# Performance work log

Measured on AMD Instinct MI355X. Metric: run time of the kernel, lower is better.

The kernel has to match this reference:

```python
import jax, jax.numpy as jnp
import numpy as np

B, L, C, H, HH, NL, O = 4096, 512, 8, 64, 128, 3, 1  # batch, time length, input/hidden/hidden_hidden chans, layers, out


def _lin(k, i, o):
    s = 1.0 / np.sqrt(i)
    return jax.random.uniform(k, (i, o), jnp.float32, -s, s)


def setup_inputs():
    key = jax.random.key(0)
    ks = jax.random.split(key, 8)
    return {
        "coeffs": jax.random.normal(ks[0], (B, L - 1, 4 * C), jnp.float32) * 0.1,
        "W_init": _lin(ks[1], C, H), "b_init": jnp.zeros((H,), jnp.float32),
        "W_in": _lin(ks[2], H, HH), "b_in": jnp.zeros((HH,), jnp.float32),
        "W_h": jnp.stack([_lin(ks[3 + i], HH, HH) for i in range(NL - 1)]),
        "b_h": jnp.zeros((NL - 1, HH), jnp.float32),
        "W_out": _lin(ks[5], HH, C * H), "b_out": jnp.zeros((C * H,), jnp.float32),
        "W_read": _lin(ks[6], H, O), "b_read": jnp.zeros((O,), jnp.float32),
    }


def _cde_func(z, W_in, b_in, W_h, b_h, W_out, b_out):
    # CDEFunc MLP: (B,H) -> (B,H,C)
    h = jax.nn.relu(z @ W_in + b_in)
    for i in range(W_h.shape[0]):
        h = jax.nn.relu(h @ W_h[i] + b_h[i])
    f = jnp.tanh(h @ W_out + b_out)
    return f.reshape(z.shape[0], H, C)


def reference(coeffs, W_init, b_init, W_in, b_in, W_h, b_h, W_out, b_out, W_read, b_read):
    # torchcde.CubicSpline coeffs layout: cat([a, b, two_c, three_d], dim=-1)
    a, bb, two_c, three_d = jnp.split(coeffs, 4, axis=-1)  # each (B, L-1, C)
    # X(interval[0]) = a of the first segment (fractional part 0)
    z = a[:, 0, :] @ W_init + b_init  # (B, H)
    # grid_points = arange(L); step size h = 1 between consecutive grid points
    bs = jnp.moveaxis(bb, 1, 0)       # (L-1, B, C)
    cs = jnp.moveaxis(two_c, 1, 0)
    ds = jnp.moveaxis(three_d, 1, 0)

    def step(z, seg):
        bn, cn, dn = seg
        deriv = lambda frac: bn + (cn + dn * frac) * frac  # dX/dt within segment
        g = lambda zz, dX: jnp.einsum(
            'bhc,bc->bh', _cde_func(zz, W_in, b_in, W_h, b_h, W_out, b_out), dX)
        third = jnp.float32(1.0 / 3.0)
        # torchdiffeq 'rk4' fixed-grid solver = Kutta's 3/8 rule (rk4_alt_step_func), h=1
        k1 = g(z, deriv(0.0))
        k2 = g(z + k1 * third, deriv(third))
        k3 = g(z + (k2 - k1 * third), deriv(2.0 * third))
        k4 = g(z + (k1 - k2 + k3), deriv(1.0))
        z = z + (k1 + 3.0 * (k2 + k3) + k4) * jnp.float32(0.125)
        return z, None

    zT, _ = jax.lax.scan(step, z, (bs, cs, ds))  # final hidden state z(T)
    return zT @ W_read + b_read  # (B, O)
```

## Files before the change

### kernel.cpp

```cpp
#include <hip/hip_runtime.h>
#include <stdint.h>

typedef short s16x8 __attribute__((ext_vector_type(8)));
typedef float f32x4 __attribute__((ext_vector_type(4)));

#define LSEG 511

static __device__ __forceinline__ uint32_t cvt_pk_bf16(float lo, float hi) {
  uint32_t r;
  asm("v_cvt_pk_bf16_f32 %0, %1, %2" : "=v"(r) : "v"(lo), "v"(hi));
  return r;
}
static __device__ __forceinline__ unsigned short f2bf(float f) {
  union { float f; uint32_t u; } v; v.f = f;
  uint32_t r = (v.u + 0x7FFFu + ((v.u >> 16) & 1u)) >> 16;
  return (unsigned short)r;
}
static __device__ __forceinline__ float dpp_xor8(float x) {
  return __int_as_float(__builtin_amdgcn_update_dpp(
      0, __float_as_int(x), 0x128, 0xF, 0xF, false));
}

__global__ __attribute__((amdgpu_flat_work_group_size(512, 512),
                          amdgpu_waves_per_eu(2, 2)))
void cde_kernel(
    const float* __restrict__ coeffs,
    const float* __restrict__ W_init, const float* __restrict__ b_init,
    const float* __restrict__ W_in,  const float* __restrict__ b_in,
    const float* __restrict__ W_h,   const float* __restrict__ b_h,
    const float* __restrict__ W_out, const float* __restrict__ b_out,
    const float* __restrict__ W_read,const float* __restrict__ b_read,
    float* __restrict__ out)
{
  __shared__ __align__(16) char H1mem[16 * 256];
  __shared__ __align__(16) char H2mem[16 * 256];
  __shared__ __align__(16) char Xmem[16 * 128];
  __shared__ float dx2[4][2][16][4];

  const int tid  = threadIdx.x;
  const int w    = tid >> 6;
  const int lane = tid & 63;
  const int lr   = lane & 15;
  const int lk   = lane >> 4;
  const int lc   = lr & 7;
  const int hp   = lr >> 3;
  const int b0   = blockIdx.x * 16;
  const int h_own = 8*w + lc;

  const float TS = 2.8853900817779268f;

  s16x8 Win_f[2], Wh0_f[4], Wh1_f[4], Wout_f[4][4];
  const int wc = 16*w + lr;
  #pragma unroll
  for (int kq = 0; kq < 2; ++kq)
    #pragma unroll
    for (int e = 0; e < 8; ++e)
      Win_f[kq][e] = (short)f2bf(W_in[(32*kq + 8*lk + e)*128 + wc]);
  #pragma unroll
  for (int kq = 0; kq < 4; ++kq)
    #pragma unroll
    for (int e = 0; e < 8; ++e) {
      Wh0_f[kq][e] = (short)f2bf(W_h[(32*kq + 8*lk + e)*128 + wc]);
      Wh1_f[kq][e] = (short)f2bf(W_h[16384 + (32*kq + 8*lk + e)*128 + wc]);
    }
  #pragma unroll
  for (int kq = 0; kq < 4; ++kq)
    #pragma unroll
    for (int nt = 0; nt < 4; ++nt) {
      const int ch = 64*w + 8*lc + 2*nt + hp;
      #pragma unroll
      for (int e = 0; e < 8; ++e)
        Wout_f[kq][nt][e] = (short)f2bf(W_out[(32*kq + 8*lk + e)*512 + ch] * TS);
    }
  const float binv = b_in[wc];
  const float bh0v = b_h[wc];
  const float bh1v = b_h[128 + wc];
  const f32x4 bin4 = {binv, binv, binv, binv};
  const f32x4 bh04 = {bh0v, bh0v, bh0v, bh0v};
  const f32x4 bh14 = {bh1v, bh1v, bh1v, bh1v};
  f32x4 bout4[4];
  #pragma unroll
  for (int nt = 0; nt < 4; ++nt) {
    const float b = b_out[64*w + 8*lc + 2*nt + hp] * TS;
    bout4[nt] = (f32x4){b, b, b, b};
  }

  const int r2  = (lr >> 2) & 1;
  const int vbHe = lr*256 + (((lk ^ lr) & 3) << 4) + (r2 << 6);
  const int vbHo = lr*256 + (((lk ^ lr) & 3) << 4) + ((1 ^ r2) << 6);
  const int vbX0 = lr*128 + ((lk ^ (lr & 7)) << 4);
  const int vbX1 = vbX0 ^ 64;
  int wbH[4];
  #pragma unroll
  for (int r = 0; r < 4; ++r) {
    const int row = 4*lk + r;
    wbH[r] = row*256 + ((((2*w + (lr >> 3)) ^ (row & 7)) << 4)) + ((lr & 7) << 1);
  }
  int wbX[2];
  #pragma unroll
  for (int j = 0; j < 2; ++j) {
    const int ro = 4*lk + 2*hp + j;
    wbX[j] = ro*128 + (((w ^ (ro & 7)) << 4)) + (lc << 1);
  }
  const int dbx = hp*256 + lk*64;

  float z0[2], zfin[2], k1r[2], k2r[2];
  {
    float Wi[8];
    #pragma unroll
    for (int c = 0; c < 8; ++c) Wi[c] = W_init[c*64 + h_own];
    const float bi = b_init[h_own];
    #pragma unroll
    for (int j = 0; j < 2; ++j) {
      const int ro = 4*lk + 2*hp + j;
      const float* a0r = &coeffs[(size_t)(b0 + ro) * (LSEG*32)];
      float s = bi;
      #pragma unroll
      for (int c = 0; c < 8; ++c) s = fmaf(a0r[c], Wi[c], s);
      z0[j] = s; zfin[j] = 0.f; k1r[j] = 0.f; k2r[j] = 0.f;
      *(unsigned short*)(Xmem + wbX[j]) = f2bf(s);
    }
  }

  float cf_b = 0.f, cf_c = 0.f, cf_d = 0.f;
  const int crow = 2*w + (lane >> 5);
  const int ccc  = (lane >> 2) & 7;
  const bool cact = (lane & 3) == 0;
  if (cact) {
    const float* cp = &coeffs[(size_t)(b0 + crow)*(LSEG*32)];
    cf_b = cp[8+ccc]; cf_c = cp[16+ccc]; cf_d = cp[24+ccc];
  }
  __syncthreads();

  #pragma unroll 1
  for (int t = 0; t < LSEG; ++t) {
    #pragma unroll
    for (int s = 0; s < 4; ++s) {
      if (s == 0 && cact) {
        const float third = 1.f/3.f, two3 = 2.f/3.f;
        const int dxo = (ccc & 1)*256 + crow*16 + (ccc >> 1)*4;
        *(float*)((char*)dx2 + dxo)        = cf_b;
        *(float*)((char*)dx2 + dxo + 512)  = fmaf(fmaf(cf_d, third, cf_c), third, cf_b);
        *(float*)((char*)dx2 + dxo + 1024) = fmaf(fmaf(cf_d, two3, cf_c), two3, cf_b);
        *(float*)((char*)dx2 + dxo + 1536) = cf_b + cf_c + cf_d;
        if (t + 1 < LSEG) {
          const float* cp = &coeffs[((size_t)(b0 + crow)*LSEG + (t+1))*32];
          cf_b = cp[8+ccc]; cf_c = cp[16+ccc]; cf_d = cp[24+ccc];
        }
      }
      {
        s16x8 a0 = *(const s16x8*)(Xmem + vbX0);
        s16x8 a1 = *(const s16x8*)(Xmem + vbX1);
        __builtin_amdgcn_s_setprio(1);
        f32x4 acc;
        acc = __builtin_amdgcn_mfma_f32_16x16x32_bf16(a0, Win_f[0], bin4, 0, 0, 0);
        acc = __builtin_amdgcn_mfma_f32_16x16x32_bf16(a1, Win_f[1], acc, 0, 0, 0);
        __builtin_amdgcn_s_setprio(0);
        #pragma unroll
        for (int r = 0; r < 4; ++r) {
          float v = fmaxf(acc[r], 0.f);
          *(unsigned short*)(H1mem + wbH[r]) = (unsigned short)cvt_pk_bf16(v, v);
        }
      }
      __syncthreads();

      {
        s16x8 a0 = *(const s16x8*)(H1mem + vbHe);
        s16x8 a1 = *(const s16x8*)(H1mem + vbHo);
        s16x8 a2 = *(const s16x8*)(H1mem + vbHe + 128);
        s16x8 a3 = *(const s16x8*)(H1mem + vbHo + 128);
        __builtin_amdgcn_s_setprio(1);
        f32x4 acc0, acc1 = {};
        acc0 = __builtin_amdgcn_mfma_f32_16x16x32_bf16(a0, Wh0_f[0], bh04, 0, 0, 0);
        acc1 = __builtin_amdgcn_mfma_f32_16x16x32_bf16(a1, Wh0_f[1], acc1, 0, 0, 0);
        acc0 = __builtin_amdgcn_mfma_f32_16x16x32_bf16(a2, Wh0_f[2], acc0, 0, 0, 0);
        acc1 = __builtin_amdgcn_mfma_f32_16x16x32_bf16(a3, Wh0_f[3], acc1, 0, 0, 0);
        __builtin_amdgcn_s_setprio(0);
        f32x4 acc = acc0 + acc1;
        #pragma unroll
        for (int r = 0; r < 4; ++r) {
          float v = fmaxf(acc[r], 0.f);
          *(unsigned short*)(H2mem + wbH[r]) = (unsigned short)cvt_pk_bf16(v, v);
        }
      }
      __syncthreads();

      {
        s16x8 a0 = *(const s16x8*)(H2mem + vbHe);
        s16x8 a1 = *(const s16x8*)(H2mem + vbHo);
        s16x8 a2 = *(const s16x8*)(H2mem + vbHe + 128);
        s16x8 a3 = *(const s16x8*)(H2mem + vbHo + 128);
        __builtin_amdgcn_s_setprio(1);
        f32x4 acc0, acc1 = {};
        acc0 = __builtin_amdgcn_mfma_f32_16x16x32_bf16(a0, Wh1_f[0], bh14, 0, 0, 0);
        acc1 = __builtin_amdgcn_mfma_f32_16x16x32_bf16(a1, Wh1_f[1], acc1, 0, 0, 0);
        acc0 = __builtin_amdgcn_mfma_f32_16x16x32_bf16(a2, Wh1_f[2], acc0, 0, 0, 0);
        acc1 = __builtin_amdgcn_mfma_f32_16x16x32_bf16(a3, Wh1_f[3], acc1, 0, 0, 0);
        __builtin_amdgcn_s_setprio(0);
        f32x4 acc = acc0 + acc1;
        #pragma unroll
        for (int r = 0; r < 4; ++r) {
          float v = fmaxf(acc[r], 0.f);
          *(unsigned short*)(H1mem + wbH[r]) = (unsigned short)cvt_pk_bf16(v, v);
        }
      }
      __syncthreads();

      {
        f32x4 dxv[4];
        #pragma unroll
        for (int r = 0; r < 4; ++r)
          dxv[r] = *(const f32x4*)((const char*)dx2 + dbx + s*512 + r*16);
        s16x8 a0 = *(const s16x8*)(H1mem + vbHe);
        s16x8 a1 = *(const s16x8*)(H1mem + vbHo);
        s16x8 a2 = *(const s16x8*)(H1mem + vbHe + 128);
        s16x8 a3 = *(const s16x8*)(H1mem + vbHo + 128);
        __builtin_amdgcn_s_setprio(1);
        f32x4 acc[4];
        #pragma unroll
        for (int nt = 0; nt < 4; ++nt)
          acc[nt] = __builtin_amdgcn_mfma_f32_16x16x32_bf16(a0, Wout_f[0][nt], bout4[nt], 0, 0, 0);
        #pragma unroll
        for (int nt = 0; nt < 4; ++nt)
          acc[nt] = __builtin_amdgcn_mfma_f32_16x16x32_bf16(a1, Wout_f[1][nt], acc[nt], 0, 0, 0);
        #pragma unroll
        for (int nt = 0; nt < 4; ++nt)
          acc[nt] = __builtin_amdgcn_mfma_f32_16x16x32_bf16(a2, Wout_f[2][nt], acc[nt], 0, 0, 0);
        #pragma unroll
        for (int nt = 0; nt < 4; ++nt)
          acc[nt] = __builtin_amdgcn_mfma_f32_16x16x32_bf16(a3, Wout_f[3][nt], acc[nt], 0, 0, 0);
        __builtin_amdgcn_s_setprio(0);
        float sums[4];
        #pragma unroll
        for (int r = 0; r < 4; ++r) {
          float sum = 0.f;
          #pragma unroll
          for (int nt = 0; nt < 4; ++nt) {
            float e2 = __builtin_amdgcn_exp2f(acc[nt][r]);
            float rr = __builtin_amdgcn_rcpf(e2 + 1.f);
            float tv = fmaf(-2.f, rr, 1.f);
            sum = fmaf(tv, dxv[r][nt], sum);
          }
          sums[r] = sum + dpp_xor8(sum);
        }
        #pragma unroll
        for (int j = 0; j < 2; ++j) {
          const float sum = sums[2*hp + j];
          float znext;
          if (s == 0) {
            k1r[j] = sum;
            zfin[j] = fmaf(0.125f, sum, z0[j]);
            znext   = fmaf(1.f/3.f, sum, z0[j]);
          } else if (s == 1) {
            k2r[j] = sum;
            zfin[j] = fmaf(0.375f, sum, zfin[j]);
            znext   = z0[j] + sum - (1.f/3.f)*k1r[j];
          } else if (s == 2) {
            zfin[j] = fmaf(0.375f, sum, zfin[j]);
            znext   = z0[j] + k1r[j] - k2r[j] + sum;
          } else {
            zfin[j] = fmaf(0.125f, sum, zfin[j]);
            znext   = zfin[j];
            z0[j]   = zfin[j];
          }
          *(unsigned short*)(Xmem + wbX[j]) = (unsigned short)cvt_pk_bf16(znext, znext);
        }
      }
      __syncthreads();
    }
  }

  float* ZF = (float*)H1mem;
  #pragma unroll
  for (int j = 0; j < 2; ++j)
    ZF[(4*lk + 2*hp + j)*64 + h_own] = z0[j];
  __syncthreads();
  if (tid < 16) {
    float acc = b_read[0];
    for (int h = 0; h < 64; ++h) acc = fmaf(ZF[tid*64 + h], W_read[h], acc);
    out[b0 + tid] = acc;
  }
}

extern "C" void kernel_launch(void* const* d_in, const int* in_sizes, int n_in,
                              void* d_out, int out_size, void* d_ws, size_t ws_size,
                              hipStream_t stream) {
  const float* coeffs = (const float*)d_in[0];
  const float* W_init = (const float*)d_in[1];
  const float* b_init = (const float*)d_in[2];
  const float* W_in   = (const float*)d_in[3];
  const float* b_in   = (const float*)d_in[4];
  const float* W_h    = (const float*)d_in[5];
  const float* b_h    = (const float*)d_in[6];
  const float* W_out  = (const float*)d_in[7];
  const float* b_out  = (const float*)d_in[8];
  const float* W_read = (const float*)d_in[9];
  const float* b_read = (const float*)d_in[10];
  float* out = (float*)d_out;

  cde_kernel<<<dim3(256), dim3(512), 0, stream>>>(
      coeffs, W_init, b_init, W_in, b_in, W_h, b_h, W_out, b_out,
      W_read, b_read, out);
}
```

Baseline: 2.828 ms.

## Swap MFMA operand order to produce transposed outputs with packed LDS stores

Swaps the A/B operands of every MFMA so weights become the row operand and activations the column operand, which transposes the output fragment layout. Each lane now holds four consecutive hidden channels of one batch row, so it writes one packed 8-byte LDS store instead of four scalar 2-byte stores, and the dX reads shrink to a single vector load. The Wout column mapping, bias vectors, swizzles and dX buffer layout are rearranged to match. The cross-lane reduction moves from a DPP xor-8 to a shuffle xor-32. RK4 state per lane grows from two to four values, with duplicated work in the upper lanes.

```diff
diff --git a/kernel.cpp b/kernel.cpp
--- a/kernel.cpp
+++ b/kernel.cpp
@@ -3,6 +3,7 @@
 
 typedef short s16x8 __attribute__((ext_vector_type(8)));
 typedef float f32x4 __attribute__((ext_vector_type(4)));
+typedef uint32_t u32x2 __attribute__((ext_vector_type(2)));
 
 #define LSEG 511
 
@@ -15,10 +16,6 @@
   union { float f; uint32_t u; } v; v.f = f;
   uint32_t r = (v.u + 0x7FFFu + ((v.u >> 16) & 1u)) >> 16;
   return (unsigned short)r;
-}
-static __device__ __forceinline__ float dpp_xor8(float x) {
-  return __int_as_float(__builtin_amdgcn_update_dpp(
-      0, __float_as_int(x), 0x128, 0xF, 0xF, false));
 }
 
 __global__ __attribute__((amdgpu_flat_work_group_size(512, 512),
@@ -35,17 +32,14 @@
   __shared__ __align__(16) char H1mem[16 * 256];
   __shared__ __align__(16) char H2mem[16 * 256];
   __shared__ __align__(16) char Xmem[16 * 128];
-  __shared__ float dx2[4][2][16][4];
+  __shared__ float dx2[4][16][8];
 
   const int tid  = threadIdx.x;
   const int w    = tid >> 6;
   const int lane = tid & 63;
   const int lr   = lane & 15;
   const int lk   = lane >> 4;
-  const int lc   = lr & 7;
-  const int hp   = lr >> 3;
   const int b0   = blockIdx.x * 16;
-  const int h_own = 8*w + lc;
 
   const float TS = 2.8853900817779268f;
 
@@ -67,58 +61,52 @@
   for (int kq = 0; kq < 4; ++kq)
     #pragma unroll
     for (int nt = 0; nt < 4; ++nt) {
-      const int ch = 64*w + 8*lc + 2*nt + hp;
+      const int ch = (8*w + 2*nt + ((lr >> 2) & 1))*8 + (lr & 3) + 4*((lr >> 3) & 1);
       #pragma unroll
       for (int e = 0; e < 8; ++e)
         Wout_f[kq][nt][e] = (short)f2bf(W_out[(32*kq + 8*lk + e)*512 + ch] * TS);
     }
-  const float binv = b_in[wc];
-  const float bh0v = b_h[wc];
-  const float bh1v = b_h[128 + wc];
-  const f32x4 bin4 = {binv, binv, binv, binv};
-  const f32x4 bh04 = {bh0v, bh0v, bh0v, bh0v};
-  const f32x4 bh14 = {bh1v, bh1v, bh1v, bh1v};
-  f32x4 bout4[4];
-  #pragma unroll
-  for (int nt = 0; nt < 4; ++nt) {
-    const float b = b_out[64*w + 8*lc + 2*nt + hp] * TS;
-    bout4[nt] = (f32x4){b, b, b, b};
-  }
-
-  const int r2  = (lr >> 2) & 1;
-  const int vbHe = lr*256 + (((lk ^ lr) & 3) << 4) + (r2 << 6);
-  const int vbHo = lr*256 + (((lk ^ lr) & 3) << 4) + ((1 ^ r2) << 6);
+  f32x4 bin4, bh04, bh14, bout4[4];
+  #pragma unroll
+  for (int r = 0; r < 4; ++r) {
+    bin4[r] = b_in[16*w + 4*lk + r];
+    bh04[r] = b_h[16*w + 4*lk + r];
+    bh14[r] = b_h[128 + 16*w + 4*lk + r];
+  }
+  #pragma unroll
+  for (int nt = 0; nt < 4; ++nt)
+    #pragma unroll
+    for (int r = 0; r < 4; ++r)
+      bout4[nt][r] = b_out[(8*w + 2*nt + (lk & 1))*8 + 4*(lk >> 1) + r] * TS;
+
+  int vb[4];
+  #pragma unroll
+  for (int kq = 0; kq < 4; ++kq)
+    vb[kq] = lr*256 + (((4*kq + lk) ^ (lr & 7)) << 4);
   const int vbX0 = lr*128 + ((lk ^ (lr & 7)) << 4);
   const int vbX1 = vbX0 ^ 64;
-  int wbH[4];
-  #pragma unroll
-  for (int r = 0; r < 4; ++r) {
-    const int row = 4*lk + r;
-    wbH[r] = row*256 + ((((2*w + (lr >> 3)) ^ (row & 7)) << 4)) + ((lr & 7) << 1);
-  }
-  int wbX[2];
-  #pragma unroll
-  for (int j = 0; j < 2; ++j) {
-    const int ro = 4*lk + 2*hp + j;
-    wbX[j] = ro*128 + (((w ^ (ro & 7)) << 4)) + (lc << 1);
-  }
-  const int dbx = hp*256 + lk*64;
-
-  float z0[2], zfin[2], k1r[2], k2r[2];
+  const int wbH = lr*256 + (((2*w + (lk >> 1)) ^ (lr & 7)) << 4) + (lk & 1)*8;
+  int wbXh[4];
+  #pragma unroll
+  for (int nt = 0; nt < 4; ++nt)
+    wbXh[nt] = lr*128 + ((w ^ (lr & 7)) << 4) + 2*(2*nt + (lk & 1));
+  const int dbx = lr*32 + (lk >> 1)*16;
+
+  float z0[4], zfin[4], k1r[4], k2r[4];
   {
-    float Wi[8];
-    #pragma unroll
-    for (int c = 0; c < 8; ++c) Wi[c] = W_init[c*64 + h_own];
-    const float bi = b_init[h_own];
-    #pragma unroll
-    for (int j = 0; j < 2; ++j) {
-      const int ro = 4*lk + 2*hp + j;
-      const float* a0r = &coeffs[(size_t)(b0 + ro) * (LSEG*32)];
-      float s = bi;
+    const float* a0r = &coeffs[(size_t)(b0 + lr) * (LSEG*32)];
+    #pragma unroll
+    for (int nt = 0; nt < 4; ++nt) {
+      const int h = 8*w + 2*nt + (lk & 1);
+      float s = b_init[h];
       #pragma unroll
-      for (int c = 0; c < 8; ++c) s = fmaf(a0r[c], Wi[c], s);
-      z0[j] = s; zfin[j] = 0.f; k1r[j] = 0.f; k2r[j] = 0.f;
-      *(unsigned short*)(Xmem + wbX[j]) = f2bf(s);
+      for (int c = 0; c < 8; ++c) s = fmaf(a0r[c], W_init[c*64 + h], s);
+      z0[nt] = s; zfin[nt] = 0.f; k1r[nt] = 0.f; k2r[nt] = 0.f;
+    }
+    if (lk < 2) {
+      #pragma unroll
+      for (int nt = 0; nt < 4; ++nt)
+        *(unsigned short*)(Xmem + wbXh[nt]) = (unsigned short)cvt_pk_bf16(z0[nt], z0[nt]);
     }
   }
 
@@ -138,11 +126,11 @@
     for (int s = 0; s < 4; ++s) {
       if (s == 0 && cact) {
         const float third = 1.f/3.f, two3 = 2.f/3.f;
-        const int dxo = (ccc & 1)*256 + crow*16 + (ccc >> 1)*4;
-        *(float*)((char*)dx2 + dxo)        = cf_b;
-        *(float*)((char*)dx2 + dxo + 512)  = fmaf(fmaf(cf_d, third, cf_c), third, cf_b);
-        *(float*)((char*)dx2 + dxo + 1024) = fmaf(fmaf(cf_d, two3, cf_c), two3, cf_b);
-        *(float*)((char*)dx2 + dxo + 1536) = cf_b + cf_c + cf_d;
+        float* dp = &dx2[0][crow][ccc];
+        dp[0]   = cf_b;
+        dp[128] = fmaf(fmaf(cf_d, third, cf_c), third, cf_b);
+        dp[256] = fmaf(fmaf(cf_d, two3, cf_c), two3, cf_b);
+        dp[384] = cf_b + cf_c + cf_d;
         if (t + 1 < LSEG) {
           const float* cp = &coeffs[((size_t)(b0 + crow)*LSEG + (t+1))*32];
           cf_b = cp[8+ccc]; cf_c = cp[16+ccc]; cf_d = cp[24+ccc];
@@ -153,117 +141,107 @@
         s16x8 a1 = *(const s16x8*)(Xmem + vbX1);
         __builtin_amdgcn_s_setprio(1);
         f32x4 acc;
-        acc = __builtin_amdgcn_mfma_f32_16x16x32_bf16(a0, Win_f[0], bin4, 0, 0, 0);
-        acc = __builtin_amdgcn_mfma_f32_16x16x32_bf16(a1, Win_f[1], acc, 0, 0, 0);
-        __builtin_amdgcn_s_setprio(0);
-        #pragma unroll
-        for (int r = 0; r < 4; ++r) {
-          float v = fmaxf(acc[r], 0.f);
-          *(unsigned short*)(H1mem + wbH[r]) = (unsigned short)cvt_pk_bf16(v, v);
-        }
-      }
-      __syncthreads();
-
-      {
-        s16x8 a0 = *(const s16x8*)(H1mem + vbHe);
-        s16x8 a1 = *(const s16x8*)(H1mem + vbHo);
-        s16x8 a2 = *(const s16x8*)(H1mem + vbHe + 128);
-        s16x8 a3 = *(const s16x8*)(H1mem + vbHo + 128);
+        acc = __builtin_amdgcn_mfma_f32_16x16x32_bf16(Win_f[0], a0, bin4, 0, 0, 0);
+        acc = __builtin_amdgcn_mfma_f32_16x16x32_bf16(Win_f[1], a1, acc, 0, 0, 0);
+        __builtin_amdgcn_s_setprio(0);
+        u32x2 pk;
+        pk[0] = cvt_pk_bf16(fmaxf(acc[0], 0.f), fmaxf(acc[1], 0.f));
+        pk[1] = cvt_pk_bf16(fmaxf(acc[2], 0.f), fmaxf(acc[3], 0.f));
+        *(u32x2*)(H1mem + wbH) = pk;
+      }
+      __syncthreads();
+
+      {
+        s16x8 a0 = *(const s16x8*)(H1mem + vb[0]);
+        s16x8 a1 = *(const s16x8*)(H1mem + vb[1]);
+        s16x8 a2 = *(const s16x8*)(H1mem + vb[2]);
+        s16x8 a3 = *(const s16x8*)(H1mem + vb[3]);
         __builtin_amdgcn_s_setprio(1);
         f32x4 acc0, acc1 = {};
-        acc0 = __builtin_amdgcn_mfma_f32_16x16x32_bf16(a0, Wh0_f[0], bh04, 0, 0, 0);
-        acc1 = __builtin_amdgcn_mfma_f32_16x16x32_bf16(a1, Wh0_f[1], acc1, 0, 0, 0);
-        acc0 = __builtin_amdgcn_mfma_f32_16x16x32_bf16(a2, Wh0_f[2], acc0, 0, 0, 0);
-        acc1 = __builtin_amdgcn_mfma_f32_16x16x32_bf16(a3, Wh0_f[3], acc1, 0, 0, 0);
+        acc0 = __builtin_amdgcn_mfma_f32_16x16x32_bf16(Wh0_f[0], a0, bh04, 0, 0, 0);
+        acc1 = __builtin_amdgcn_mfma_f32_16x16x32_bf16(Wh0_f[1], a1, acc1, 0, 0, 0);
+        acc0 = __builtin_amdgcn_mfma_f32_16x16x32_bf16(Wh0_f[2], a2, acc0, 0, 0, 0);
+        acc1 = __builtin_amdgcn_mfma_f32_16x16x32_bf16(Wh0_f[3], a3, acc1, 0, 0, 0);
         __builtin_amdgcn_s_setprio(0);
         f32x4 acc = acc0 + acc1;
-        #pragma unroll
-        for (int r = 0; r < 4; ++r) {
-          float v = fmaxf(acc[r], 0.f);
-          *(unsigned short*)(H2mem + wbH[r]) = (unsigned short)cvt_pk_bf16(v, v);
-        }
-      }
-      __syncthreads();
-
-      {
-        s16x8 a0 = *(const s16x8*)(H2mem + vbHe);
-        s16x8 a1 = *(const s16x8*)(H2mem + vbHo);
-        s16x8 a2 = *(const s16x8*)(H2mem + vbHe + 128);
-        s16x8 a3 = *(const s16x8*)(H2mem + vbHo + 128);
+        u32x2 pk;
+        pk[0] = cvt_pk_bf16(fmaxf(acc[0], 0.f), fmaxf(acc[1], 0.f));
+        pk[1] = cvt_pk_bf16(fmaxf(acc[2], 0.f), fmaxf(acc[3], 0.f));
+        *(u32x2*)(H2mem + wbH) = pk;
+      }
+      __syncthreads();
+
+      {
+        s16x8 a0 = *(const s16x8*)(H2mem + vb[0]);
+        s16x8 a1 = *(const s16x8*)(H2mem + vb[1]);
+        s16x8 a2 = *(const s16x8*)(H2mem + vb[2]);
+        s16x8 a3 = *(const s16x8*)(H2mem + vb[3]);
         __builtin_amdgcn_s_setprio(1);
         f32x4 acc0, acc1 = {};
-        acc0 = __builtin_amdgcn_mfma_f32_16x16x32_bf16(a0, Wh1_f[0], bh14, 0, 0, 0);
-        acc1 = __builtin_amdgcn_mfma_f32_16x16x32_bf16(a1, Wh1_f[1], acc1, 0, 0, 0);
-        acc0 = __builtin_amdgcn_mfma_f32_16x16x32_bf16(a2, Wh1_f[2], acc0, 0, 0, 0);
-        acc1 = __builtin_amdgcn_mfma_f32_16x16x32_bf16(a3, Wh1_f[3], acc1, 0, 0, 0);
+        acc0 = __builtin_amdgcn_mfma_f32_16x16x32_bf16(Wh1_f[0], a0, bh14, 0, 0, 0);
+        acc1 = __builtin_amdgcn_mfma_f32_16x16x32_bf16(Wh1_f[1], a1, acc1, 0, 0, 0);
+        acc0 = __builtin_amdgcn_mfma_f32_16x16x32_bf16(Wh1_f[2], a2, acc0, 0, 0, 0);
+        acc1 = __builtin_amdgcn_mfma_f32_16x16x32_bf16(Wh1_f[3], a3, acc1, 0, 0, 0);
         __builtin_amdgcn_s_setprio(0);
         f32x4 acc = acc0 + acc1;
-        #pragma unroll
-        for (int r = 0; r < 4; ++r) {
-          float v = fmaxf(acc[r], 0.f);
-          *(unsigned short*)(H1mem + wbH[r]) = (unsigned short)cvt_pk_bf16(v, v);
-        }
-      }
-      __syncthreads();
-
-      {
-        f32x4 dxv[4];
-        #pragma unroll
-        for (int r = 0; r < 4; ++r)
-          dxv[r] = *(const f32x4*)((const char*)dx2 + dbx + s*512 + r*16);
-        s16x8 a0 = *(const s16x8*)(H1mem + vbHe);
-        s16x8 a1 = *(const s16x8*)(H1mem + vbHo);
-        s16x8 a2 = *(const s16x8*)(H1mem + vbHe + 128);
-        s16x8 a3 = *(const s16x8*)(H1mem + vbHo + 128);
+        u32x2 pk;
+        pk[0] = cvt_pk_bf16(fmaxf(acc[0], 0.f), fmaxf(acc[1], 0.f));
+        pk[1] = cvt_pk_bf16(fmaxf(acc[2], 0.f), fmaxf(acc[3], 0.f));
+        *(u32x2*)(H1mem + wbH) = pk;
+      }
+      __syncthreads();
+
+      {
+        f32x4 dxv = *(const f32x4*)((const char*)dx2 + s*512 + dbx);
+        s16x8 a0 = *(const s16x8*)(H1mem + vb[0]);
+        s16x8 a1 = *(const s16x8*)(H1mem + vb[1]);
+        s16x8 a2 = *(const s16x8*)(H1mem + vb[2]);
+        s16x8 a3 = *(const s16x8*)(H1mem + vb[3]);
         __builtin_amdgcn_s_setprio(1);
         f32x4 acc[4];
         #pragma unroll
         for (int nt = 0; nt < 4; ++nt)
-          acc[nt] = __builtin_amdgcn_mfma_f32_16x16x32_bf16(a0, Wout_f[0][nt], bout4[nt], 0, 0, 0);
-        #pragma unroll
-        for (int nt = 0; nt < 4; ++nt)
-          acc[nt] = __builtin_amdgcn_mfma_f32_16x16x32_bf16(a1, Wout_f[1][nt], acc[nt], 0, 0, 0);
-        #pragma unroll
-        for (int nt = 0; nt < 4; ++nt)
-          acc[nt] = __builtin_amdgcn_mfma_f32_16x16x32_bf16(a2, Wout_f[2][nt], acc[nt], 0, 0, 0);
-        #pragma unroll
-        for (int nt = 0; nt < 4; ++nt)
-          acc[nt] = __builtin_amdgcn_mfma_f32_16x16x32_bf16(a3, Wout_f[3][nt], acc[nt], 0, 0, 0);
-        __builtin_amdgcn_s_setprio(0);
-        float sums[4];
-        #pragma unroll
-        for (int r = 0; r < 4; ++r) {
+          acc[nt] = __builtin_amdgcn_mfma_f32_16x16x32_bf16(Wout_f[0][nt], a0, bout4[nt], 0, 0, 0);
+        #pragma unroll
+        for (int nt = 0; nt < 4; ++nt)
+          acc[nt] = __builtin_amdgcn_mfma_f32_16x16x32_bf16(Wout_f[1][nt], a1, acc[nt], 0, 0, 0);
+        #pragma unroll
+        for (int nt = 0; nt < 4; ++nt)
+          acc[nt] = __builtin_amdgcn_mfma_f32_16x16x32_bf16(Wout_f[2][nt], a2, acc[nt], 0, 0, 0);
+        #pragma unroll
+        for (int nt = 0; nt < 4; ++nt)
+          acc[nt] = __builtin_amdgcn_mfma_f32_16x16x32_bf16(Wout_f[3][nt], a3, acc[nt], 0, 0, 0);
+        __builtin_amdgcn_s_setprio(0);
+        #pragma unroll
+        for (int nt = 0; nt < 4; ++nt) {
           float sum = 0.f;
           #pragma unroll
-          for (int nt = 0; nt < 4; ++nt) {
+          for (int r = 0; r < 4; ++r) {
             float e2 = __builtin_amdgcn_exp2f(acc[nt][r]);
             float rr = __builtin_amdgcn_rcpf(e2 + 1.f);
             float tv = fmaf(-2.f, rr, 1.f);
-            sum = fmaf(tv, dxv[r][nt], sum);
+            sum = fmaf(tv, dxv[r], sum);
           }
-          sums[r] = sum + dpp_xor8(sum);
-        }
-        #pragma unroll
-        for (int j = 0; j < 2; ++j) {
-          const float sum = sums[2*hp + j];
+          sum += __shfl_xor(sum, 32);
           float znext;
           if (s == 0) {
-            k1r[j] = sum;
-            zfin[j] = fmaf(0.125f, sum, z0[j]);
-            znext   = fmaf(1.f/3.f, sum, z0[j]);
+            k1r[nt] = sum;
+            zfin[nt] = fmaf(0.125f, sum, z0[nt]);
+            znext    = fmaf(1.f/3.f, sum, z0[nt]);
           } else if (s == 1) {
-            k2r[j] = sum;
-            zfin[j] = fmaf(0.375f, sum, zfin[j]);
-            znext   = z0[j] + sum - (1.f/3.f)*k1r[j];
+            k2r[nt] = sum;
+            zfin[nt] = fmaf(0.375f, sum, zfin[nt]);
+            znext    = z0[nt] + sum - (1.f/3.f)*k1r[nt];
           } else if (s == 2) {
-            zfin[j] = fmaf(0.375f, sum, zfin[j]);
-            znext   = z0[j] + k1r[j] - k2r[j] + sum;
+            zfin[nt] = fmaf(0.375f, sum, zfin[nt]);
+            znext    = z0[nt] + k1r[nt] - k2r[nt] + sum;
           } else {
-            zfin[j] = fmaf(0.125f, sum, zfin[j]);
-            znext   = zfin[j];
-            z0[j]   = zfin[j];
+            zfin[nt] = fmaf(0.125f, sum, zfin[nt]);
+            znext    = zfin[nt];
+            z0[nt]   = zfin[nt];
           }
-          *(unsigned short*)(Xmem + wbX[j]) = (unsigned short)cvt_pk_bf16(znext, znext);
+          if (lk < 2)
+            *(unsigned short*)(Xmem + wbXh[nt]) = (unsigned short)cvt_pk_bf16(znext, znext);
         }
       }
       __syncthreads();
@@ -271,9 +249,11 @@
   }
 
   float* ZF = (float*)H1mem;
-  #pragma unroll
-  for (int j = 0; j < 2; ++j)
-    ZF[(4*lk + 2*hp + j)*64 + h_own] = z0[j];
+  if (lk < 2) {
+    #pragma unroll
+    for (int nt = 0; nt < 4; ++nt)
+      ZF[lr*64 + 8*w + 2*nt + (lk & 1)] = z0[nt];
+  }
   __syncthreads();
   if (tid < 16) {
     float acc = b_read[0];
```

Result: no change. 2.867 ms (+1.4%).
